# Kernel optimization log

Measured on AMD Instinct MI355X. Metric: run time of the kernel, lower is better.

Reference implementation:

```python
import jax, jax.numpy as jnp
import numpy as np

NUM_ATOM, NUM_CHIRAL = 120, 4
B, N, E = 8, 12500, 80000
D, H = 128, 128  # emb_dim_gnn, hidden_gnn
NEG_SLOPE = 0.2


def setup_inputs() -> dict:
    key = jax.random.key(0)
    ks = jax.random.split(key, 9)
    return {
        "atom_idx": jax.random.randint(ks[0], (B, N), 0, NUM_ATOM, dtype=jnp.int32),
        "chiral_idx": jax.random.randint(ks[1], (B, N), 0, NUM_CHIRAL, dtype=jnp.int32),
        "edge_index": jax.random.randint(ks[2], (B, 2, E), 0, N, dtype=jnp.int32),
        "emb_atom": jax.random.normal(ks[3], (NUM_ATOM, D), jnp.float32) * 0.1,
        "emb_chiral": jax.random.normal(ks[4], (NUM_CHIRAL, D), jnp.float32) * 0.1,
        "W1": jax.random.normal(ks[5], (D, H), jnp.float32) * (1.0 / np.sqrt(D)),
        "b1": jnp.zeros((H,), jnp.float32),
        "W2": jax.random.normal(ks[6], (H, H), jnp.float32) * (1.0 / np.sqrt(H)),
        "b2": jnp.zeros((H,), jnp.float32),
    }


def _gcn_conv(h, src, dst, W, b):
    """PyG GCNConv: linear -> sym-normalized aggregation with self-loops -> bias."""
    n = h.shape[0]
    h = h @ W  # [N, out]
    # degree on destination including self-loop weight 1
    deg = jnp.ones((n,), h.dtype).at[dst].add(1.0)
    dis = jax.lax.rsqrt(deg)  # deg^{-1/2}; deg >= 1 so no inf
    coef = (dis[src] * dis[dst])[:, None]  # [E,1] edge norm
    agg = jnp.zeros_like(h).at[dst].add(h[src] * coef)  # scatter-add messages
    agg = agg + h * (dis * dis)[:, None]  # self-loop contribution norm = deg_i^{-1}
    return agg + b


def _forward_one(atom, chiral, edge, emb_atom, emb_chiral, W1, b1, W2, b2):
    h = emb_atom[atom] + emb_chiral[chiral]  # [N, D]
    src, dst = edge[0], edge[1]
    h = jax.nn.leaky_relu(_gcn_conv(h, src, dst, W1, b1), NEG_SLOPE)
    h = jax.nn.leaky_relu(_gcn_conv(h, src, dst, W2, b2), NEG_SLOPE)
    return h.mean(axis=0)  # graph-level mean pool -> [H]


def reference(atom_idx, chiral_idx, edge_index, emb_atom, emb_chiral, W1, b1, W2, b2):
    f = jax.vmap(_forward_one, in_axes=(0, 0, 0, None, None, None, None, None, None))
    return f(atom_idx, chiral_idx, edge_index, emb_atom, emb_chiral, W1, b1, W2, b2)  # [B, H]
```

## Files before the change

kernel.cpp:

```cpp
#include <hip/hip_runtime.h>

#define B_ 8
#define N_ 12500
#define E_ 80000
#define D_ 128
#define CAP_ 32

typedef __attribute__((ext_vector_type(8))) short bf16x8;
typedef __attribute__((ext_vector_type(4))) float f32x4;

__device__ inline unsigned short f2bf(float x) {
  unsigned int u = __float_as_uint(x);
  return (unsigned short)((u + 0x7FFFu + ((u >> 16) & 1u)) >> 16);
}
__device__ inline float bflo(unsigned int u) { return __uint_as_float(u << 16); }
__device__ inline float bfhi(unsigned int u) { return __uint_as_float(u & 0xFFFF0000u); }

__global__ __launch_bounds__(256) void k_zero(int* cnt, float* part) {
  int i = blockIdx.x * 256 + threadIdx.x;
  if (i < B_ * N_) cnt[i] = 0;
  if (i < 32 * B_ * D_) part[i] = 0.f;
}

__global__ __launch_bounds__(256) void k_fill_ell(
    const int* __restrict__ edge, const int* __restrict__ atom,
    const int* __restrict__ chiral, int* __restrict__ cnt,
    unsigned short* __restrict__ ell_src, unsigned short* __restrict__ ell_cmb) {
  int i = blockIdx.x * 256 + threadIdx.x;
  if (i >= B_ * E_) return;
  int b = i / E_, e = i - b * E_;
  const int* eb = edge + (size_t)b * 2 * E_;
  int src = eb[e];
  int dst = eb[E_ + e];
  int comb = atom[b * N_ + src] * 4 + chiral[b * N_ + src];
  int slot = atomicAdd(&cnt[b * N_ + dst], 1);
  if (slot < CAP_) {
    size_t idx = (size_t)(b * N_ + dst) * CAP_ + slot;
    ell_src[idx] = (unsigned short)src;
    ell_cmb[idx] = (unsigned short)comb;
  }
}

__global__ __launch_bounds__(256) void k_dis(const int* __restrict__ cnt,
                                             float* __restrict__ dis) {
  int i = blockIdx.x * 256 + threadIdx.x;
  if (i < B_ * N_) dis[i] = rsqrtf(1.0f + (float)cnt[i]);
}

__global__ __launch_bounds__(128) void k_tc(const float* __restrict__ ea,
                                            const float* __restrict__ ec,
                                            const float* __restrict__ W1,
                                            float* __restrict__ TC) {
  int r = blockIdx.x, j = threadIdx.x;
  int a = r >> 2, c = r & 3;
  float acc = 0.f;
#pragma unroll 8
  for (int k = 0; k < D_; ++k)
    acc += (ea[a * D_ + k] + ec[c * D_ + k]) * W1[k * D_ + j];
  TC[r * D_ + j] = acc;
}

__global__ __launch_bounds__(256) void k_wcvt(const float* __restrict__ W,
                                              unsigned short* __restrict__ Wb) {
  int i = blockIdx.x * 256 + threadIdx.x;
  if (i >= D_ * D_) return;
  int k = i >> 7, c = i & 127;
  Wb[c * D_ + k] = f2bf(W[i]);
}

__global__ __launch_bounds__(256) void k_gather1(
    const unsigned short* __restrict__ ell_src,
    const unsigned short* __restrict__ ell_cmb, const int* __restrict__ cnt,
    const float* __restrict__ dis, const float* __restrict__ TC,
    const int* __restrict__ atom, const int* __restrict__ chiral,
    const float* __restrict__ bias, unsigned short* __restrict__ H1) {
  int b = blockIdx.x & 7;
  int rb = blockIdx.x >> 3;
  int w = threadIdx.x >> 6;
  int r = rb * 4 + w;
  int lane = threadIdx.x & 63;
  int row = b * N_ + r;
  int deg = min(cnt[row], CAP_);
  float dr = dis[row];
  size_t ebase = (size_t)row * CAP_ + (lane & 31);
  int srcl = ell_src[ebase];
  int cmbl = ell_cmb[ebase];
  float dsl = dis[b * N_ + min(srcl, N_ - 1)];
  float coefv = (lane < deg) ? dsl * dr : 0.f;
  const float2* TC2 = (const float2*)TC;
  float2 acc = {0.f, 0.f};
  for (int j0 = 0; j0 < deg; j0 += 8) {
#pragma unroll
    for (int jj = 0; jj < 8; ++jj) {
      float cj = __shfl(coefv, j0 + jj);
      int comb = __shfl(cmbl, j0 + jj);
      if (cj != 0.f) {
        float2 v = TC2[comb * 64 + lane];
        acc.x += v.x * cj;
        acc.y += v.y * cj;
      }
    }
  }
  int combr = atom[row] * 4 + chiral[row];
  float2 h = TC2[combr * 64 + lane];
  float dd = dr * dr;
  float ox = acc.x + h.x * dd + bias[lane * 2 + 0];
  float oy = acc.y + h.y * dd + bias[lane * 2 + 1];
  ox = (ox >= 0.f) ? ox : 0.2f * ox;
  oy = (oy >= 0.f) ? oy : 0.2f * oy;
  unsigned int pk = (unsigned int)f2bf(ox) | ((unsigned int)f2bf(oy) << 16);
  *(unsigned int*)&H1[(size_t)row * D_ + lane * 2] = pk;
}

__global__ __launch_bounds__(256) void k_gemm2(
    const unsigned short* __restrict__ A, const unsigned short* __restrict__ Wb,
    unsigned short* __restrict__ out) {
  int b = blockIdx.x & 7;
  int blk = blockIdx.x >> 3;
  int t = threadIdx.x;
  int wave = t >> 6, lane = t & 63;
  int row0 = blk * 64 + wave * 16;
  int arow = row0 + (lane & 15);
  if (arow >= N_) arow = N_ - 1;
  const unsigned short* Ar = A + ((size_t)b * N_ + arow) * D_;
  int kh = (lane >> 4) * 8;
  bf16x8 af[4];
#pragma unroll
  for (int kc = 0; kc < 4; ++kc) af[kc] = *(const bf16x8*)&Ar[kc * 32 + kh];
  f32x4 acc[8];
#pragma unroll
  for (int ct = 0; ct < 8; ++ct) acc[ct] = (f32x4){0.f, 0.f, 0.f, 0.f};
#pragma unroll
  for (int ct = 0; ct < 8; ++ct) {
    int c = ct * 16 + (lane & 15);
#pragma unroll
    for (int kc = 0; kc < 4; ++kc) {
      bf16x8 bfr = *(const bf16x8*)&Wb[c * D_ + kc * 32 + kh];
      acc[ct] =
          __builtin_amdgcn_mfma_f32_16x16x32_bf16(af[kc], bfr, acc[ct], 0, 0, 0);
    }
  }
  int ro = row0 + (lane >> 4) * 4;
  int co = lane & 15;
#pragma unroll
  for (int ct = 0; ct < 8; ++ct)
#pragma unroll
    for (int rg = 0; rg < 4; ++rg) {
      int r = ro + rg;
      if (r < N_)
        out[((size_t)b * N_ + r) * D_ + ct * 16 + co] = f2bf(acc[ct][rg]);
    }
}

__global__ __launch_bounds__(256) void k_gather2(
    const unsigned short* __restrict__ ell_src, const int* __restrict__ cnt,
    const float* __restrict__ dis, const unsigned short* __restrict__ H2,
    const float* __restrict__ bias, float* __restrict__ part) {
  __shared__ float red[4][128];
  int b = blockIdx.x & 7;
  int rb = blockIdx.x >> 3;
  int w = threadIdx.x >> 6;
  int r = rb * 4 + w;
  int lane = threadIdx.x & 63;
  int row = b * N_ + r;
  int deg = min(cnt[row], CAP_);
  float dr = dis[row];
  int srcl = ell_src[(size_t)row * CAP_ + (lane & 31)];
  float dsl = dis[b * N_ + min(srcl, N_ - 1)];
  float coefv = (lane < deg) ? dsl * dr : 0.f;
  const unsigned short* Hb = H2 + (size_t)b * N_ * D_;
  float2 acc = {0.f, 0.f};
  for (int j0 = 0; j0 < deg; j0 += 8) {
#pragma unroll
    for (int jj = 0; jj < 8; ++jj) {
      float cj = __shfl(coefv, j0 + jj);
      int s = __shfl(srcl, j0 + jj);
      if (cj != 0.f) {
        unsigned int u = *(const unsigned int*)&Hb[(size_t)s * D_ + lane * 2];
        acc.x += bflo(u) * cj;
        acc.y += bfhi(u) * cj;
      }
    }
  }
  float dd = dr * dr;
  unsigned int uh = *(const unsigned int*)&Hb[(size_t)r * D_ + lane * 2];
  float ox = acc.x + bflo(uh) * dd + bias[lane * 2 + 0];
  float oy = acc.y + bfhi(uh) * dd + bias[lane * 2 + 1];
  ox = (ox >= 0.f) ? ox : 0.2f * ox;
  oy = (oy >= 0.f) ? oy : 0.2f * oy;
  red[w][lane * 2] = ox;
  red[w][lane * 2 + 1] = oy;
  __syncthreads();
  if (w == 0) {
    float sx = red[0][lane * 2] + red[1][lane * 2] + red[2][lane * 2] +
               red[3][lane * 2];
    float sy = red[0][lane * 2 + 1] + red[1][lane * 2 + 1] +
               red[2][lane * 2 + 1] + red[3][lane * 2 + 1];
    float* pp = part + (size_t)(rb & 31) * (B_ * D_) + b * D_;
    atomicAdd(&pp[lane * 2 + 0], sx);
    atomicAdd(&pp[lane * 2 + 1], sy);
  }
}

__global__ __launch_bounds__(256) void k_outred(const float* __restrict__ part,
                                                float* __restrict__ out) {
  int i = blockIdx.x * 256 + threadIdx.x;
  if (i >= B_ * D_) return;
  float s = 0.f;
#pragma unroll
  for (int p = 0; p < 32; ++p) s += part[p * (B_ * D_) + i];
  out[i] = s * (1.0f / (float)N_);
}

extern "C" void kernel_launch(void* const* d_in, const int* in_sizes, int n_in,
                              void* d_out, int out_size, void* d_ws,
                              size_t ws_size, hipStream_t stream) {
  const int* atom = (const int*)d_in[0];
  const int* chiral = (const int*)d_in[1];
  const int* edge = (const int*)d_in[2];
  const float* emb_atom = (const float*)d_in[3];
  const float* emb_chiral = (const float*)d_in[4];
  const float* W1 = (const float*)d_in[5];
  const float* b1 = (const float*)d_in[6];
  const float* W2 = (const float*)d_in[7];
  const float* b2 = (const float*)d_in[8];
  float* out = (float*)d_out;

  char* w = (char*)d_ws;
  float* dis = (float*)(w + (0ll << 20));
  int* cnt = (int*)(w + (1ll << 20));
  unsigned short* ell_src = (unsigned short*)(w + (2ll << 20));
  unsigned short* ell_cmb = (unsigned short*)(w + (9ll << 20));
  float* TC = (float*)(w + (16ll << 20));
  unsigned short* Wb = (unsigned short*)(w + (17ll << 20));
  float* part = (float*)(w + (18ll << 20));
  unsigned short* H1 = (unsigned short*)(w + (20ll << 20));
  unsigned short* H2 = (unsigned short*)(w + (48ll << 20));

  int gBN = (B_ * N_ + 255) / 256;
  int gBE = (B_ * E_ + 255) / 256;
  k_zero<<<gBN, 256, 0, stream>>>(cnt, part);
  k_fill_ell<<<gBE, 256, 0, stream>>>(edge, atom, chiral, cnt, ell_src,
                                      ell_cmb);
  k_dis<<<gBN, 256, 0, stream>>>(cnt, dis);
  k_tc<<<480, 128, 0, stream>>>(emb_atom, emb_chiral, W1, TC);
  k_wcvt<<<(D_ * D_ + 255) / 256, 256, 0, stream>>>(W2, Wb);

  int gGather = (N_ / 4) * B_;
  int gGemm = ((N_ + 63) / 64) * B_;
  k_gather1<<<gGather, 256, 0, stream>>>(ell_src, ell_cmb, cnt, dis, TC, atom,
                                         chiral, b1, H1);
  k_gemm2<<<gGemm, 256, 0, stream>>>(H1, Wb, H2);
  k_gather2<<<gGather, 256, 0, stream>>>(ell_src, cnt, dis, H2, b2, part);
  k_outred<<<(B_ * D_ + 255) / 256, 256, 0, stream>>>(part, out);
}
```

Baseline: 274.1 us.

## Precompute packed fp16 edge coefficients in ELL and merge weight prep kernels

Adds a k_coef pass that turns the ELL entries into packed 32-bit words holding an fp16 edge coefficient together with the combo index (for layer 1) or the source index (for layer 2). This removes the per-row dis gathers and shuffles from both gather kernels, which now read the packed words with wave-uniform loads in unrolled groups of four. The TC and W2-conversion kernels are merged into one launch. In exchange it adds an extra pass over the whole padded ELL array and reads padded zero entries, and the coefficients are rounded to fp16.

```diff
diff --git a/kernel.cpp b/kernel.cpp
--- a/kernel.cpp
+++ b/kernel.cpp
@@ -1,4 +1,5 @@
 #include <hip/hip_runtime.h>
+#include <hip/hip_fp16.h>
 
 #define B_ 8
 #define N_ 12500
@@ -15,6 +16,9 @@
 }
 __device__ inline float bflo(unsigned int u) { return __uint_as_float(u << 16); }
 __device__ inline float bfhi(unsigned int u) { return __uint_as_float(u & 0xFFFF0000u); }
+__device__ inline float h2f(unsigned int hi16) {
+  return __half2float(__ushort_as_half((unsigned short)hi16));
+}
 
 __global__ __launch_bounds__(256) void k_zero(int* cnt, float* part) {
   int i = blockIdx.x * 256 + threadIdx.x;
@@ -25,7 +29,7 @@
 __global__ __launch_bounds__(256) void k_fill_ell(
     const int* __restrict__ edge, const int* __restrict__ atom,
     const int* __restrict__ chiral, int* __restrict__ cnt,
-    unsigned short* __restrict__ ell_src, unsigned short* __restrict__ ell_cmb) {
+    unsigned int* __restrict__ ellA) {
   int i = blockIdx.x * 256 + threadIdx.x;
   if (i >= B_ * E_) return;
   int b = i / E_, e = i - b * E_;
@@ -34,11 +38,9 @@
   int dst = eb[E_ + e];
   int comb = atom[b * N_ + src] * 4 + chiral[b * N_ + src];
   int slot = atomicAdd(&cnt[b * N_ + dst], 1);
-  if (slot < CAP_) {
-    size_t idx = (size_t)(b * N_ + dst) * CAP_ + slot;
-    ell_src[idx] = (unsigned short)src;
-    ell_cmb[idx] = (unsigned short)comb;
-  }
+  if (slot < CAP_)
+    ellA[(size_t)(b * N_ + dst) * CAP_ + slot] =
+        (unsigned int)src | ((unsigned int)comb << 14);
 }
 
 __global__ __launch_bounds__(256) void k_dis(const int* __restrict__ cnt,
@@ -47,61 +49,82 @@
   if (i < B_ * N_) dis[i] = rsqrtf(1.0f + (float)cnt[i]);
 }
 
-__global__ __launch_bounds__(128) void k_tc(const float* __restrict__ ea,
-                                            const float* __restrict__ ec,
-                                            const float* __restrict__ W1,
-                                            float* __restrict__ TC) {
-  int r = blockIdx.x, j = threadIdx.x;
-  int a = r >> 2, c = r & 3;
-  float acc = 0.f;
+__global__ __launch_bounds__(256) void k_coef(const int* __restrict__ cnt,
+                                              const float* __restrict__ dis,
+                                              unsigned int* __restrict__ ellA,
+                                              unsigned int* __restrict__ ellB) {
+  int i = blockIdx.x * 256 + threadIdx.x;
+  if (i >= B_ * N_ * CAP_) return;
+  int row = i >> 5;
+  int slot = i & 31;
+  int b = row / N_;
+  int deg = min(cnt[row], CAP_);
+  unsigned int a = 0, bb = 0;
+  if (slot < deg) {
+    unsigned int t = ellA[i];
+    int src = t & 0x3FFF;
+    int cmb = t >> 14;
+    float coef = dis[b * N_ + src] * dis[row];
+    unsigned int cf = (unsigned int)__half_as_ushort(__float2half_rn(coef));
+    a = (unsigned int)cmb | (cf << 16);
+    bb = (unsigned int)src | (cf << 16);
+  }
+  ellA[i] = a;
+  ellB[i] = bb;
+}
+
+__global__ __launch_bounds__(128) void k_tcw(const float* __restrict__ ea,
+                                             const float* __restrict__ ec,
+                                             const float* __restrict__ W1,
+                                             const float* __restrict__ W2,
+                                             float* __restrict__ TC,
+                                             unsigned short* __restrict__ Wb) {
+  int blk = blockIdx.x;
+  if (blk < 480) {
+    int j = threadIdx.x;
+    int a = blk >> 2, c = blk & 3;
+    float acc = 0.f;
 #pragma unroll 8
-  for (int k = 0; k < D_; ++k)
-    acc += (ea[a * D_ + k] + ec[c * D_ + k]) * W1[k * D_ + j];
-  TC[r * D_ + j] = acc;
-}
-
-__global__ __launch_bounds__(256) void k_wcvt(const float* __restrict__ W,
-                                              unsigned short* __restrict__ Wb) {
-  int i = blockIdx.x * 256 + threadIdx.x;
-  if (i >= D_ * D_) return;
-  int k = i >> 7, c = i & 127;
-  Wb[c * D_ + k] = f2bf(W[i]);
+    for (int k = 0; k < D_; ++k)
+      acc += (ea[a * D_ + k] + ec[c * D_ + k]) * W1[k * D_ + j];
+    TC[blk * D_ + j] = acc;
+  } else {
+    int i = (blk - 480) * 128 + threadIdx.x;
+    if (i < D_ * D_) {
+      int k = i >> 7, c = i & 127;
+      Wb[c * D_ + k] = f2bf(W2[i]);
+    }
+  }
 }
 
 __global__ __launch_bounds__(256) void k_gather1(
-    const unsigned short* __restrict__ ell_src,
-    const unsigned short* __restrict__ ell_cmb, const int* __restrict__ cnt,
+    const unsigned int* __restrict__ ellA, const int* __restrict__ cnt,
     const float* __restrict__ dis, const float* __restrict__ TC,
     const int* __restrict__ atom, const int* __restrict__ chiral,
     const float* __restrict__ bias, unsigned short* __restrict__ H1) {
   int b = blockIdx.x & 7;
   int rb = blockIdx.x >> 3;
-  int w = threadIdx.x >> 6;
-  int r = rb * 4 + w;
+  int r = rb * 4 + (threadIdx.x >> 6);
   int lane = threadIdx.x & 63;
-  int row = b * N_ + r;
-  int deg = min(cnt[row], CAP_);
-  float dr = dis[row];
-  size_t ebase = (size_t)row * CAP_ + (lane & 31);
-  int srcl = ell_src[ebase];
-  int cmbl = ell_cmb[ebase];
-  float dsl = dis[b * N_ + min(srcl, N_ - 1)];
-  float coefv = (lane < deg) ? dsl * dr : 0.f;
+  int row = __builtin_amdgcn_readfirstlane(b * N_ + r);
+  int deg = __builtin_amdgcn_readfirstlane(min(cnt[row], CAP_));
+  int base = row * CAP_;
   const float2* TC2 = (const float2*)TC;
   float2 acc = {0.f, 0.f};
-  for (int j0 = 0; j0 < deg; j0 += 8) {
-#pragma unroll
-    for (int jj = 0; jj < 8; ++jj) {
-      float cj = __shfl(coefv, j0 + jj);
-      int comb = __shfl(cmbl, j0 + jj);
-      if (cj != 0.f) {
-        float2 v = TC2[comb * 64 + lane];
-        acc.x += v.x * cj;
-        acc.y += v.y * cj;
-      }
+  int nb = (deg + 3) >> 2;
+  for (int bi = 0; bi < nb; ++bi) {
+#pragma unroll
+    for (int k = 0; k < 4; ++k) {
+      unsigned int t = ellA[base + bi * 4 + k];
+      float cj = h2f(t >> 16);
+      int cb = (int)(t & 0xFFFFu);
+      float2 v = TC2[cb * 64 + lane];
+      acc.x += v.x * cj;
+      acc.y += v.y * cj;
     }
   }
   int combr = atom[row] * 4 + chiral[row];
+  float dr = dis[row];
   float2 h = TC2[combr * 64 + lane];
   float dd = dr * dr;
   float ox = acc.x + h.x * dd + bias[lane * 2 + 0];
@@ -153,7 +176,7 @@
 }
 
 __global__ __launch_bounds__(256) void k_gather2(
-    const unsigned short* __restrict__ ell_src, const int* __restrict__ cnt,
+    const unsigned int* __restrict__ ellB, const int* __restrict__ cnt,
     const float* __restrict__ dis, const unsigned short* __restrict__ H2,
     const float* __restrict__ bias, float* __restrict__ part) {
   __shared__ float red[4][128];
@@ -162,28 +185,26 @@
   int w = threadIdx.x >> 6;
   int r = rb * 4 + w;
   int lane = threadIdx.x & 63;
-  int row = b * N_ + r;
-  int deg = min(cnt[row], CAP_);
-  float dr = dis[row];
-  int srcl = ell_src[(size_t)row * CAP_ + (lane & 31)];
-  float dsl = dis[b * N_ + min(srcl, N_ - 1)];
-  float coefv = (lane < deg) ? dsl * dr : 0.f;
+  int row = __builtin_amdgcn_readfirstlane(b * N_ + r);
+  int deg = __builtin_amdgcn_readfirstlane(min(cnt[row], CAP_));
+  int base = row * CAP_;
   const unsigned short* Hb = H2 + (size_t)b * N_ * D_;
   float2 acc = {0.f, 0.f};
-  for (int j0 = 0; j0 < deg; j0 += 8) {
-#pragma unroll
-    for (int jj = 0; jj < 8; ++jj) {
-      float cj = __shfl(coefv, j0 + jj);
-      int s = __shfl(srcl, j0 + jj);
-      if (cj != 0.f) {
-        unsigned int u = *(const unsigned int*)&Hb[(size_t)s * D_ + lane * 2];
-        acc.x += bflo(u) * cj;
-        acc.y += bfhi(u) * cj;
-      }
-    }
-  }
+  int nb = (deg + 3) >> 2;
+  for (int bi = 0; bi < nb; ++bi) {
+#pragma unroll
+    for (int k = 0; k < 4; ++k) {
+      unsigned int t = ellB[base + bi * 4 + k];
+      float cj = h2f(t >> 16);
+      int s = (int)(t & 0xFFFFu);
+      unsigned int u = *(const unsigned int*)&Hb[(size_t)s * D_ + lane * 2];
+      acc.x += bflo(u) * cj;
+      acc.y += bfhi(u) * cj;
+    }
+  }
+  float dr = dis[row];
   float dd = dr * dr;
-  unsigned int uh = *(const unsigned int*)&Hb[(size_t)r * D_ + lane * 2];
+  unsigned int uh = *(const unsigned int*)&Hb[(size_t)(row - b * N_) * D_ + lane * 2];
   float ox = acc.x + bflo(uh) * dd + bias[lane * 2 + 0];
   float oy = acc.y + bfhi(uh) * dd + bias[lane * 2 + 1];
   ox = (ox >= 0.f) ? ox : 0.2f * ox;
@@ -229,28 +250,28 @@
   char* w = (char*)d_ws;
   float* dis = (float*)(w + (0ll << 20));
   int* cnt = (int*)(w + (1ll << 20));
-  unsigned short* ell_src = (unsigned short*)(w + (2ll << 20));
-  unsigned short* ell_cmb = (unsigned short*)(w + (9ll << 20));
-  float* TC = (float*)(w + (16ll << 20));
-  unsigned short* Wb = (unsigned short*)(w + (17ll << 20));
-  float* part = (float*)(w + (18ll << 20));
-  unsigned short* H1 = (unsigned short*)(w + (20ll << 20));
-  unsigned short* H2 = (unsigned short*)(w + (48ll << 20));
+  unsigned int* ellA = (unsigned int*)(w + (2ll << 20));
+  unsigned int* ellB = (unsigned int*)(w + (16ll << 20));
+  float* TC = (float*)(w + (29ll << 20));
+  unsigned short* Wb = (unsigned short*)(w + (30ll << 20));
+  float* part = (float*)(w + (31ll << 20));
+  unsigned short* H1 = (unsigned short*)(w + (32ll << 20));
+  unsigned short* H2 = (unsigned short*)(w + (60ll << 20));
 
   int gBN = (B_ * N_ + 255) / 256;
   int gBE = (B_ * E_ + 255) / 256;
   k_zero<<<gBN, 256, 0, stream>>>(cnt, part);
-  k_fill_ell<<<gBE, 256, 0, stream>>>(edge, atom, chiral, cnt, ell_src,
-                                      ell_cmb);
+  k_fill_ell<<<gBE, 256, 0, stream>>>(edge, atom, chiral, cnt, ellA);
   k_dis<<<gBN, 256, 0, stream>>>(cnt, dis);
-  k_tc<<<480, 128, 0, stream>>>(emb_atom, emb_chiral, W1, TC);
-  k_wcvt<<<(D_ * D_ + 255) / 256, 256, 0, stream>>>(W2, Wb);
+  k_coef<<<(B_ * N_ * CAP_ + 255) / 256, 256, 0, stream>>>(cnt, dis, ellA,
+                                                           ellB);
+  k_tcw<<<608, 128, 0, stream>>>(emb_atom, emb_chiral, W1, W2, TC, Wb);
 
   int gGather = (N_ / 4) * B_;
   int gGemm = ((N_ + 63) / 64) * B_;
-  k_gather1<<<gGather, 256, 0, stream>>>(ell_src, ell_cmb, cnt, dis, TC, atom,
-                                         chiral, b1, H1);
+  k_gather1<<<gGather, 256, 0, stream>>>(ellA, cnt, dis, TC, atom, chiral, b1,
+                                         H1);
   k_gemm2<<<gGemm, 256, 0, stream>>>(H1, Wb, H2);
-  k_gather2<<<gGather, 256, 0, stream>>>(ell_src, cnt, dis, H2, b2, part);
+  k_gather2<<<gGather, 256, 0, stream>>>(ellB, cnt, dis, H2, b2, part);
   k_outred<<<(B_ * D_ + 255) / 256, 256, 0, stream>>>(part, out);
 }
```

Measured after the change: 228.9 us. 1.2x faster.
